# Performance work log

Hardware: AMD Instinct MI355X
Metric: run time of the kernel (lower is better)

The kernel has to match this reference:

```python
import jax, jax.numpy as jnp
import numpy as np

N, D, H = 16384, 128, 512
C = 1.0          # curvature c_in
EPS_GIN = 0.0    # GIN epsilon
MIN_NORM = 1e-7


def _arcosh(z):
    z = jnp.clip(z, 1.0 + MIN_NORM, None)
    return jnp.log(z + jnp.sqrt(z * z - 1.0))


def exp_map_zero(u, c):
    # hyperboloid exp at origin; tangent 'time' coord u[...,0] is ignored
    sqrtK = 1.0 / jnp.sqrt(c)
    x = u[..., 1:]
    n = jnp.clip(jnp.linalg.norm(x, axis=-1, keepdims=True), MIN_NORM, None)
    theta = n / sqrtK
    return jnp.concatenate(
        [sqrtK * jnp.cosh(theta), sqrtK * jnp.sinh(theta) * x / n], axis=-1)


def log_map_zero(p, c):
    # hyperboloid log at origin; result has zero 'time' coord
    sqrtK = 1.0 / jnp.sqrt(c)
    y = p[..., 1:]
    n = jnp.clip(jnp.linalg.norm(y, axis=-1, keepdims=True), MIN_NORM, None)
    theta = _arcosh(p[..., :1] / sqrtK)
    return jnp.concatenate(
        [jnp.zeros_like(theta), sqrtK * theta * y / n], axis=-1)


def setup_inputs() -> dict:
    key = jax.random.key(0)
    k1, k2, k3, k4 = jax.random.split(key, 4)
    x = jax.random.normal(k1, (N, D), dtype=jnp.float32)
    adj = jax.random.uniform(k2, (N, N), dtype=jnp.float32) / N  # row-normalized-ish
    W1 = jax.random.normal(k3, (D, H), dtype=jnp.float32) * (1.0 / np.sqrt(D))
    b1 = jnp.zeros((H,), dtype=jnp.float32)
    W2 = jax.random.normal(k4, (H, D), dtype=jnp.float32) * (1.0 / np.sqrt(H))
    b2 = jnp.zeros((D,), dtype=jnp.float32)
    return {"x": x, "adj": adj, "W1": W1, "b1": b1, "W2": W2, "b2": b2}


def reference(x, adj, W1, b1, W2, b2):
    # 1) lift features onto hyperboloid
    h = exp_map_zero(x, C)                       # [N, D]
    # 2) LorentzAgg (no attention): aggregate in tangent space at origin
    agg = exp_map_zero(adj @ log_map_zero(h, C), C)   # [N, D]
    # 3) GIN combine in tangent space: log(out) + (1+eps)*log(x_r), then exp
    out = exp_map_zero(log_map_zero(agg, C) + (1.0 + EPS_GIN) * log_map_zero(h, C), C)
    # 4) GIN MLP
    t = jax.nn.relu(out @ W1 + b1) @ W2 + b2     # [N, D]
    return t
```

## Files before the change

### kernel.cpp

```cpp
#include <hip/hip_runtime.h>

#define GN 16384
#define GD 128
#define GH 512
#define GK 16384

#define SPLITS 2
#define SKK (GK / SPLITS)
#define BM 64
#define BK 64

typedef __attribute__((ext_vector_type(8))) short s8v;
typedef __attribute__((ext_vector_type(4))) float f4v;
typedef __attribute__((ext_vector_type(4))) int   i4v;

#define AS1 __attribute__((address_space(1)))
#define AS3 __attribute__((address_space(3)))

static __device__ inline unsigned short f2bf(float f) {
  union { float f; unsigned u; } a; a.f = f;
  unsigned r = a.u + 0x7fffu + ((a.u >> 16) & 1u);
  return (unsigned short)(r >> 16);
}

static __device__ inline unsigned cvtpk(float lo, float hi) {
  unsigned r;
  asm("v_cvt_pk_bf16_f32 %0, %1, %2" : "=v"(r) : "v"(lo), "v"(hi));
  return r;
}

static __device__ inline float waveAllSum(float v) {
  #pragma unroll
  for (int off = 32; off; off >>= 1) v += __shfl_xor(v, off);
  return v;
}

__global__ void k_logmap(const float* __restrict__ x, float* __restrict__ Lf) {
  int row  = (blockIdx.x << 2) + (threadIdx.x >> 6);
  int lane = threadIdx.x & 63;
  size_t base = ((size_t)row << 7) + (lane << 1);
  float2 v = *(const float2*)(x + base);
  float a0 = (lane == 0) ? 0.f : v.x;
  float a1 = v.y;
  float n = fmaxf(sqrtf(waveAllSum(a0*a0 + a1*a1)), 1e-7f);
  float sh = sinhf(n), ch = coshf(n);
  float y0 = sh * a0 / n, y1 = sh * a1 / n;
  float ny = fmaxf(sqrtf(waveAllSum(y0*y0 + y1*y1)), 1e-7f);
  float z  = fmaxf(ch, 1.f + 1e-7f);
  float th = logf(z + sqrtf(z*z - 1.f));
  float l0 = th * y0 / ny;
  float l1 = th * y1 / ny;
  if (lane == 0) l0 = 0.f;
  *(float2*)(Lf + base) = make_float2(l0, l1);
}

__global__ void k_tconv(const float* __restrict__ src, unsigned short* __restrict__ dst,
                        int NR, int NC) {
  __shared__ float tile[64][65];
  const int r0 = blockIdx.x << 6;
  const int c0 = blockIdx.y << 6;
  const int t  = threadIdx.x;
  const int r  = t >> 2;
  const int cg = (t & 3) << 4;
  const float* s = src + (size_t)(r0 + r) * NC + c0 + cg;
  #pragma unroll
  for (int j = 0; j < 4; ++j) {
    float4 f = ((const float4*)s)[j];
    tile[r][cg + 4*j + 0] = f.x;
    tile[r][cg + 4*j + 1] = f.y;
    tile[r][cg + 4*j + 2] = f.z;
    tile[r][cg + 4*j + 3] = f.w;
  }
  __syncthreads();
  s8v o0, o1;
  #pragma unroll
  for (int j = 0; j < 8; ++j) o0[j] = (short)f2bf(tile[cg + j][r]);
  #pragma unroll
  for (int j = 0; j < 8; ++j) o1[j] = (short)f2bf(tile[cg + 8 + j][r]);
  unsigned short* d = dst + (size_t)(c0 + r) * NR + r0 + cg;
  *(s8v*)d = o0;
  *((s8v*)d + 1) = o1;
}

#define ASZ (BM * BK * 4)
#define BSZ (128 * BK * 2)
#define BUFSZ (ASZ + BSZ)
__global__ __launch_bounds__(512) void k_gemm(const float* __restrict__ adj,
    const unsigned short* __restrict__ Lt, float* __restrict__ Mpart) {
  __shared__ __align__(16) char lds[2 * BUFSZ];
  const int tid  = threadIdx.x;
  const int lane = tid & 63, wid = tid >> 6;
  const int wr = wid >> 2, wn = wid & 3;
  const int l15 = lane & 15, lhi = (lane >> 4) << 3;
  const int bid = blockIdx.x;
  const int split = bid & 1, rowblk = bid >> 1;
  const size_t blockRow = (size_t)rowblk * BM;
  const size_t k0 = (size_t)split * SKK;

  f4v acc[2][2];
  #pragma unroll
  for (int m = 0; m < 2; ++m)
    #pragma unroll
    for (int n = 0; n < 2; ++n) acc[m][n] = (f4v){0.f, 0.f, 0.f, 0.f};

  const int rA = tid >> 4, gA = tid & 15;
  const float* aSrc = adj + (blockRow + rA) * (size_t)GK + k0
                      + (size_t)((gA ^ (rA & 7)) << 2);
  const int rB = tid >> 3, gB = tid & 7;
  const unsigned short* bSrc = Lt + (size_t)rB * GK + k0
                               + (size_t)((gB ^ (rB & 7)) << 3);

  const int NIT = SKK / BK;

#define STAGE(c, itv)                                                          \
  {                                                                            \
    const float*          ap = aSrc + (size_t)(itv) * BK;                      \
    const unsigned short* bp = bSrc + (size_t)(itv) * BK;                      \
    char* ab = lds + (c) * BUFSZ;                                              \
    char* bb = lds + (c) * BUFSZ + ASZ;                                        \
    _Pragma("unroll")                                                          \
    for (int j = 0; j < 2; ++j)                                                \
      __builtin_amdgcn_global_load_lds(                                        \
        (const AS1 void*)(ap + (size_t)j * 32 * GK),                           \
        (AS3 void*)(ab + ((tid + j * 512) << 4)), 16, 0, 0);                   \
    _Pragma("unroll")                                                          \
    for (int j = 0; j < 2; ++j)                                                \
      __builtin_amdgcn_global_load_lds(                                        \
        (const AS1 void*)(bp + (size_t)j * 64 * GK),                           \
        (AS3 void*)(bb + ((tid + j * 512) << 4)), 16, 0, 0);                   \
  }

#define COMPUTE(c)                                                             \
  {                                                                            \
    const char* ab = lds + (c) * BUFSZ;                                        \
    const char* bb = lds + (c) * BUFSZ + ASZ;                                  \
    _Pragma("unroll")                                                          \
    for (int ks = 0; ks < 2; ++ks) {                                           \
      s8v bfr[2];                                                              \
      _Pragma("unroll")                                                        \
      for (int n = 0; n < 2; ++n) {                                            \
        int rowb = 32*wn + 16*n + l15;                                         \
        int gb   = (4*ks + (lhi >> 3)) ^ (rowb & 7);                           \
        bfr[n] = *(const s8v*)(bb + rowb * 128 + (gb << 4));                   \
      }                                                                        \
      _Pragma("unroll")                                                        \
      for (int m = 0; m < 2; ++m) {                                            \
        int rowa = 32*wr + 16*m + l15;                                         \
        int ga0  = 8*ks + (lhi >> 2);                                          \
        int sw   = rowa & 7;                                                   \
        f4v x0 = *(const f4v*)(ab + rowa * 256 + ((ga0       ^ sw) << 4));     \
        f4v x1 = *(const f4v*)(ab + rowa * 256 + (((ga0 + 1) ^ sw) << 4));     \
        union { unsigned u[4]; s8v v; } ua;                                    \
        ua.u[0] = cvtpk(x0[0], x0[1]);                                         \
        ua.u[1] = cvtpk(x0[2], x0[3]);                                         \
        ua.u[2] = cvtpk(x1[0], x1[1]);                                         \
        ua.u[3] = cvtpk(x1[2], x1[3]);                                         \
        acc[m][0] = __builtin_amdgcn_mfma_f32_16x16x32_bf16(ua.v, bfr[0], acc[m][0], 0, 0, 0); \
        acc[m][1] = __builtin_amdgcn_mfma_f32_16x16x32_bf16(ua.v, bfr[1], acc[m][1], 0, 0, 0); \
      }                                                                        \
    }                                                                          \
  }

  int cur = 0;
  STAGE(0, 0);
  STAGE(1, 1);

  for (int it = 0; it < NIT - 1; ++it) {
    asm volatile("s_waitcnt vmcnt(4)" ::: "memory");
    __builtin_amdgcn_s_barrier();
    COMPUTE(cur);
    __builtin_amdgcn_s_barrier();
    if (it + 2 < NIT) STAGE(cur, it + 2);
    cur ^= 1;
  }
  asm volatile("s_waitcnt vmcnt(0)" ::: "memory");
  __builtin_amdgcn_s_barrier();
  COMPUTE(cur);
#undef STAGE
#undef COMPUTE

  float* mp = Mpart + (size_t)split * GN * GD;
  #pragma unroll
  for (int m = 0; m < 2; ++m)
    #pragma unroll
    for (int n = 0; n < 2; ++n) {
      size_t r0 = blockRow + 32*wr + 16*m + ((lane >> 4) << 2);
      int    c0 = 32*wn + 16*n + l15;
      #pragma unroll
      for (int j = 0; j < 4; ++j)
        mp[(r0 + j) * GD + c0] = acc[m][n][j];
    }
}

__global__ void k_maps(const float* __restrict__ Mp, const float* __restrict__ Lf,
                       unsigned short* __restrict__ outB) {
  int row  = (blockIdx.x << 2) + (threadIdx.x >> 6);
  int lane = threadIdx.x & 63;
  size_t base = ((size_t)row << 7) + (lane << 1);
  const size_t PS = (size_t)GN * GD;
  float2 m0 = *(const float2*)(Mp + base);
  float2 m1 = *(const float2*)(Mp + PS + base);
  float mvx = m0.x + m1.x;
  float mvy = m0.y + m1.y;
  float2 lv = *(const float2*)(Lf + base);
  float v0 = (lane == 0) ? 0.f : mvx;
  float v1 = mvy;
  float nv = fmaxf(sqrtf(waveAllSum(v0*v0 + v1*v1)), 1e-7f);
  float ch = coshf(nv), sh = sinhf(nv);
  float g0 = sh * v0 / nv, g1 = sh * v1 / nv;
  float ny = fmaxf(sqrtf(waveAllSum(g0*g0 + g1*g1)), 1e-7f);
  float z  = fmaxf(ch, 1.f + 1e-7f);
  float th = logf(z + sqrtf(z*z - 1.f));
  float la0 = th * g0 / ny, la1 = th * g1 / ny;
  float s0 = la0 + lv.x, s1 = la1 + lv.y;
  if (lane == 0) s0 = 0.f;
  float ns  = fmaxf(sqrtf(waveAllSum(s0*s0 + s1*s1)), 1e-7f);
  float ch2 = coshf(ns), sh2 = sinhf(ns);
  float o0 = sh2 * s0 / ns, o1 = sh2 * s1 / ns;
  if (lane == 0) o0 = ch2;
  unsigned pack = (unsigned)f2bf(o0) | ((unsigned)f2bf(o1) << 16);
  *(unsigned*)(outB + base) = pack;
}

#define PAD1 136
#define PADH 520
__global__ __launch_bounds__(256, 2) void k_mlp(const unsigned short* __restrict__ outB,
    const unsigned short* __restrict__ W1t, const float* __restrict__ b1,
    const unsigned short* __restrict__ W2t, const float* __restrict__ b2,
    float* __restrict__ Tout) {
  __shared__ __align__(16) short sA[32 * PAD1];
  __shared__ __align__(16) short sH[32 * PADH];
  const int tid  = threadIdx.x;
  const int lane = tid & 63, wc = tid >> 6;
  const int row0 = blockIdx.x << 5;

  {
    const int r = tid >> 3, cg = (tid & 7) << 4;
    const unsigned short* src = outB + (size_t)(row0 + r) * GD + cg;
    i4v v0 = ((const i4v*)src)[0];
    i4v v1 = ((const i4v*)src)[1];
    *(i4v*)&sA[r * PAD1 + cg]     = v0;
    *(i4v*)&sA[r * PAD1 + cg + 8] = v1;
  }
  __syncthreads();

  f4v acc1[2][8];
  #pragma unroll
  for (int mi = 0; mi < 2; ++mi)
    #pragma unroll
    for (int ni = 0; ni < 8; ++ni) acc1[mi][ni] = (f4v){0.f,0.f,0.f,0.f};

  const int afr = (lane & 15) * PAD1 + ((lane >> 4) << 3);
  #pragma unroll
  for (int kk = 0; kk < 4; ++kk) {
    s8v a0 = *(const s8v*)&sA[afr + kk*32];
    s8v a1 = *(const s8v*)&sA[afr + 16*PAD1 + kk*32];
    #pragma unroll
    for (int ni = 0; ni < 8; ++ni) {
      const unsigned short* bp = W1t + (size_t)(128*wc + 16*ni + (lane & 15)) * GD
                                 + ((lane >> 4) << 3) + kk*32;
      s8v b = *(const s8v*)bp;
      acc1[0][ni] = __builtin_amdgcn_mfma_f32_16x16x32_bf16(a0, b, acc1[0][ni], 0, 0, 0);
      acc1[1][ni] = __builtin_amdgcn_mfma_f32_16x16x32_bf16(a1, b, acc1[1][ni], 0, 0, 0);
    }
  }
  #pragma unroll
  for (int ni = 0; ni < 8; ++ni) {
    int col = 128*wc + 16*ni + (lane & 15);
    float bb = b1[col];
    #pragma unroll
    for (int mi = 0; mi < 2; ++mi) {
      #pragma unroll
      for (int j = 0; j < 4; ++j) {
        int row = 16*mi + ((lane >> 4) << 2) + j;
        float v = fmaxf(acc1[mi][ni][j] + bb, 0.f);
        sH[row * PADH + col] = (short)f2bf(v);
      }
    }
  }
  __syncthreads();

  f4v acc2[2][2];
  #pragma unroll
  for (int mi = 0; mi < 2; ++mi)
    #pragma unroll
    for (int ni = 0; ni < 2; ++ni) acc2[mi][ni] = (f4v){0.f,0.f,0.f,0.f};

  const int hfr = (lane & 15) * PADH + ((lane >> 4) << 3);
  #pragma unroll
  for (int kk = 0; kk < 16; ++kk) {
    s8v a0 = *(const s8v*)&sH[hfr + kk*32];
    s8v a1 = *(const s8v*)&sH[hfr + 16*PADH + kk*32];
    #pragma unroll
    for (int ni = 0; ni < 2; ++ni) {
      const unsigned short* bp = W2t + (size_t)(32*wc + 16*ni + (lane & 15)) * GH
                                 + ((lane >> 4) << 3) + kk*32;
      s8v b = *(const s8v*)bp;
      acc2[0][ni] = __builtin_amdgcn_mfma_f32_16x16x32_bf16(a0, b, acc2[0][ni], 0, 0, 0);
      acc2[1][ni] = __builtin_amdgcn_mfma_f32_16x16x32_bf16(a1, b, acc2[1][ni], 0, 0, 0);
    }
  }
  #pragma unroll
  for (int mi = 0; mi < 2; ++mi)
    #pragma unroll
    for (int ni = 0; ni < 2; ++ni) {
      int c0 = 32*wc + 16*ni + (lane & 15);
      float bb = b2[c0];
      size_t r0 = row0 + 16*mi + ((lane >> 4) << 2);
      #pragma unroll
      for (int j = 0; j < 4; ++j)
        Tout[(r0 + j) * GD + c0] = acc2[mi][ni][j] + bb;
    }
}

extern "C" void kernel_launch(void* const* d_in, const int* in_sizes, int n_in,
                              void* d_out, int out_size, void* d_ws, size_t ws_size,
                              hipStream_t stream) {
  const float* x   = (const float*)d_in[0];
  const float* adj = (const float*)d_in[1];
  const float* W1  = (const float*)d_in[2];
  const float* b1  = (const float*)d_in[3];
  const float* W2  = (const float*)d_in[4];
  const float* b2  = (const float*)d_in[5];
  float* Tout = (float*)d_out;

  char* ws = (char*)d_ws;
  float*          Lf    = (float*)ws;
  unsigned short* Lt    = (unsigned short*)(ws + (8u  << 20));
  float*          Mpart = (float*)(ws + (12u << 20));
  unsigned short* outB  = (unsigned short*)(ws + (28u << 20));
  unsigned short* W1t   = (unsigned short*)(ws + (32u << 20));
  unsigned short* W2t   = (unsigned short*)(ws + (32u << 20) + (128u << 10));

  k_logmap <<<GN / 4, 256, 0, stream>>>(x, Lf);
  k_tconv  <<<dim3(GK / 64, GD / 64), 256, 0, stream>>>(Lf, Lt, GN, GD);
  k_tconv  <<<dim3(GD / 64, GH / 64), 256, 0, stream>>>(W1, W1t, GD, GH);
  k_tconv  <<<dim3(GH / 64, GD / 64), 256, 0, stream>>>(W2, W2t, GH, GD);
  k_gemm   <<<(GN / BM) * SPLITS, 512, 0, stream>>>(adj, Lt, Mpart);
  k_maps   <<<GN / 4, 256, 0, stream>>>(Mpart, Lf, outB);
  k_mlp    <<<GN / 32, 256, 0, stream>>>(outB, W1t, b1, W2t, b2, Tout);
}
```

Baseline: 281.4 us.

## Halve GEMM K-tile and use triple-buffered LDS pipeline with one barrier per step

The adjacency GEMM K-tile shrinks from 64 to 32 and the LDS ring grows from two buffers to three. Each iteration now issues the next stage's loads before computing, so the second barrier per iteration can be dropped. The swizzle patterns for the A and B tiles are reworked to fit the narrower rows. The aim is to cut barrier stalls and overlap loads with MFMA better, at the cost of twice as many iterations and less data in flight per load.

```diff
diff --git a/kernel.cpp b/kernel.cpp
--- a/kernel.cpp
+++ b/kernel.cpp
@@ -8,7 +8,7 @@
 #define SPLITS 2
 #define SKK (GK / SPLITS)
 #define BM 64
-#define BK 64
+#define BK 32
 
 typedef __attribute__((ext_vector_type(8))) short s8v;
 typedef __attribute__((ext_vector_type(4))) float f4v;
@@ -87,11 +87,11 @@
 #define BUFSZ (ASZ + BSZ)
 __global__ __launch_bounds__(512) void k_gemm(const float* __restrict__ adj,
     const unsigned short* __restrict__ Lt, float* __restrict__ Mpart) {
-  __shared__ __align__(16) char lds[2 * BUFSZ];
+  __shared__ __align__(16) char lds[3 * BUFSZ];
   const int tid  = threadIdx.x;
   const int lane = tid & 63, wid = tid >> 6;
   const int wr = wid >> 2, wn = wid & 3;
-  const int l15 = lane & 15, lhi = (lane >> 4) << 3;
+  const int l15 = lane & 15, hi = lane >> 4;
   const int bid = blockIdx.x;
   const int split = bid & 1, rowblk = bid >> 1;
   const size_t blockRow = (size_t)rowblk * BM;
@@ -103,12 +103,13 @@
     #pragma unroll
     for (int n = 0; n < 2; ++n) acc[m][n] = (f4v){0.f, 0.f, 0.f, 0.f};
 
-  const int rA = tid >> 4, gA = tid & 15;
+  const int rA = tid >> 3, gA = tid & 7;
   const float* aSrc = adj + (blockRow + rA) * (size_t)GK + k0
                       + (size_t)((gA ^ (rA & 7)) << 2);
-  const int rB = tid >> 3, gB = tid & 7;
+  const int rB = tid >> 2, gB = tid & 3;
+  const int swB0 = (rB ^ (rB >> 2)) & 3;
   const unsigned short* bSrc = Lt + (size_t)rB * GK + k0
-                               + (size_t)((gB ^ (rB & 7)) << 3);
+                               + (size_t)((gB ^ swB0) << 3);
 
   const int NIT = SKK / BK;
 
@@ -118,64 +119,52 @@
     const unsigned short* bp = bSrc + (size_t)(itv) * BK;                      \
     char* ab = lds + (c) * BUFSZ;                                              \
     char* bb = lds + (c) * BUFSZ + ASZ;                                        \
-    _Pragma("unroll")                                                          \
-    for (int j = 0; j < 2; ++j)                                                \
-      __builtin_amdgcn_global_load_lds(                                        \
-        (const AS1 void*)(ap + (size_t)j * 32 * GK),                           \
-        (AS3 void*)(ab + ((tid + j * 512) << 4)), 16, 0, 0);                   \
-    _Pragma("unroll")                                                          \
-    for (int j = 0; j < 2; ++j)                                                \
-      __builtin_amdgcn_global_load_lds(                                        \
-        (const AS1 void*)(bp + (size_t)j * 64 * GK),                           \
-        (AS3 void*)(bb + ((tid + j * 512) << 4)), 16, 0, 0);                   \
+    __builtin_amdgcn_global_load_lds((const AS1 void*)ap,                      \
+        (AS3 void*)(ab + (tid << 4)), 16, 0, 0);                               \
+    __builtin_amdgcn_global_load_lds((const AS1 void*)bp,                      \
+        (AS3 void*)(bb + (tid << 4)), 16, 0, 0);                               \
   }
 
 #define COMPUTE(c)                                                             \
   {                                                                            \
     const char* ab = lds + (c) * BUFSZ;                                        \
     const char* bb = lds + (c) * BUFSZ + ASZ;                                  \
+    s8v bfr[2];                                                                \
     _Pragma("unroll")                                                          \
-    for (int ks = 0; ks < 2; ++ks) {                                           \
-      s8v bfr[2];                                                              \
-      _Pragma("unroll")                                                        \
-      for (int n = 0; n < 2; ++n) {                                            \
-        int rowb = 32*wn + 16*n + l15;                                         \
-        int gb   = (4*ks + (lhi >> 3)) ^ (rowb & 7);                           \
-        bfr[n] = *(const s8v*)(bb + rowb * 128 + (gb << 4));                   \
-      }                                                                        \
-      _Pragma("unroll")                                                        \
-      for (int m = 0; m < 2; ++m) {                                            \
-        int rowa = 32*wr + 16*m + l15;                                         \
-        int ga0  = 8*ks + (lhi >> 2);                                          \
-        int sw   = rowa & 7;                                                   \
-        f4v x0 = *(const f4v*)(ab + rowa * 256 + ((ga0       ^ sw) << 4));     \
-        f4v x1 = *(const f4v*)(ab + rowa * 256 + (((ga0 + 1) ^ sw) << 4));     \
-        union { unsigned u[4]; s8v v; } ua;                                    \
-        ua.u[0] = cvtpk(x0[0], x0[1]);                                         \
-        ua.u[1] = cvtpk(x0[2], x0[3]);                                         \
-        ua.u[2] = cvtpk(x1[0], x1[1]);                                         \
-        ua.u[3] = cvtpk(x1[2], x1[3]);                                         \
-        acc[m][0] = __builtin_amdgcn_mfma_f32_16x16x32_bf16(ua.v, bfr[0], acc[m][0], 0, 0, 0); \
-        acc[m][1] = __builtin_amdgcn_mfma_f32_16x16x32_bf16(ua.v, bfr[1], acc[m][1], 0, 0, 0); \
-      }                                                                        \
+    for (int n = 0; n < 2; ++n) {                                              \
+      int rowb = 32*wn + 16*n + l15;                                           \
+      int gb   = hi ^ ((rowb ^ (rowb >> 2)) & 3);                              \
+      bfr[n] = *(const s8v*)(bb + rowb * 64 + (gb << 4));                      \
     }                                                                          \
-  }
-
-  int cur = 0;
+    _Pragma("unroll")                                                          \
+    for (int m = 0; m < 2; ++m) {                                              \
+      int rowa = 32*wr + 16*m + l15;                                           \
+      int ga0  = 2*hi;                                                         \
+      int sw   = rowa & 7;                                                     \
+      f4v x0 = *(const f4v*)(ab + rowa * 128 + ((ga0       ^ sw) << 4));       \
+      f4v x1 = *(const f4v*)(ab + rowa * 128 + (((ga0 + 1) ^ sw) << 4));       \
+      union { unsigned u[4]; s8v v; } ua;                                      \
+      ua.u[0] = cvtpk(x0[0], x0[1]);                                           \
+      ua.u[1] = cvtpk(x0[2], x0[3]);                                           \
+      ua.u[2] = cvtpk(x1[0], x1[1]);                                           \
+      ua.u[3] = cvtpk(x1[2], x1[3]);                                           \
+      acc[m][0] = __builtin_amdgcn_mfma_f32_16x16x32_bf16(ua.v, bfr[0], acc[m][0], 0, 0, 0); \
+      acc[m][1] = __builtin_amdgcn_mfma_f32_16x16x32_bf16(ua.v, bfr[1], acc[m][1], 0, 0, 0); \
+    }                                                                          \
+  }
+
+  int c0 = 0, c1 = 1, c2 = 2;
   STAGE(0, 0);
   STAGE(1, 1);
 
-  for (int it = 0; it < NIT - 1; ++it) {
-    asm volatile("s_waitcnt vmcnt(4)" ::: "memory");
+  for (int it = 0; it < NIT; ++it) {
+    if (it < NIT - 1) asm volatile("s_waitcnt vmcnt(2)" ::: "memory");
+    else              asm volatile("s_waitcnt vmcnt(0)" ::: "memory");
     __builtin_amdgcn_s_barrier();
-    COMPUTE(cur);
-    __builtin_amdgcn_s_barrier();
-    if (it + 2 < NIT) STAGE(cur, it + 2);
-    cur ^= 1;
-  }
-  asm volatile("s_waitcnt vmcnt(0)" ::: "memory");
-  __builtin_amdgcn_s_barrier();
-  COMPUTE(cur);
+    if (it + 2 < NIT) STAGE(c2, it + 2);
+    COMPUTE(c0);
+    int t = c0; c0 = c1; c1 = c2; c2 = t;
+  }
 #undef STAGE
 #undef COMPUTE
 
@@ -184,11 +173,11 @@
   for (int m = 0; m < 2; ++m)
     #pragma unroll
     for (int n = 0; n < 2; ++n) {
-      size_t r0 = blockRow + 32*wr + 16*m + ((lane >> 4) << 2);
-      int    c0 = 32*wn + 16*n + l15;
+      size_t r0 = blockRow + 32*wr + 16*m + (hi << 2);
+      int    c0e = 32*wn + 16*n + l15;
       #pragma unroll
       for (int j = 0; j < 4; ++j)
-        mp[(r0 + j) * GD + c0] = acc[m][n][j];
+        mp[(r0 + j) * GD + c0e] = acc[m][n][j];
     }
 }
 
```

Result: slower. 316.4 us (+12.5%).
